# Kernel tuning notes

Measured on AMD Instinct MI355X. Metric: run time of the kernel, lower is better.

The kernel has to match this reference:

```python
import jax, jax.numpy as jnp
import numpy as np

B, S, E = 2, 2048, 1024
H, HKV = 16, 4
D = E // H          # head_dim = 64
REP = H // HKV      # kv repeat factor = 4


def setup_inputs() -> dict:
    key = jax.random.key(0)
    ks = jax.random.split(key, 9)
    std = 0.02
    x = jax.random.normal(ks[0], (B, S, E), dtype=jnp.float32)
    # causal mask: True means masked (upper triangle, strictly above diagonal)
    mask = jnp.triu(jnp.ones((S, S), dtype=bool), k=1)
    wq_w = jax.random.normal(ks[1], (E, E), dtype=jnp.float32) * std
    wq_b = jax.random.normal(ks[2], (E,), dtype=jnp.float32) * std
    wk_w = jax.random.normal(ks[3], (HKV * D, E), dtype=jnp.float32) * std
    wk_b = jax.random.normal(ks[4], (HKV * D,), dtype=jnp.float32) * std
    wv_w = jax.random.normal(ks[5], (HKV * D, E), dtype=jnp.float32) * std
    wv_b = jax.random.normal(ks[6], (HKV * D,), dtype=jnp.float32) * std
    wo_w = jax.random.normal(ks[7], (E, E), dtype=jnp.float32) * std
    wo_b = jax.random.normal(ks[8], (E,), dtype=jnp.float32) * std
    return {"x": x, "mask": mask, "wq_w": wq_w, "wq_b": wq_b,
            "wk_w": wk_w, "wk_b": wk_b, "wv_w": wv_w, "wv_b": wv_b,
            "wo_w": wo_w, "wo_b": wo_b}


def reference(x, mask, wq_w, wq_b, wk_w, wk_b, wv_w, wv_b, wo_w, wo_b):
    b, s, e = x.shape
    # projections (torch Linear: x @ W.T + b)
    q = x @ wq_w.T + wq_b                       # [B,S,E]
    k = x @ wk_w.T + wk_b                       # [B,S,HKV*D]
    v = x @ wv_w.T + wv_b
    # q grouped by kv head: [B, HKV, REP, S, D]; k/v: [B, HKV, S, D]
    q = q.reshape(b, s, HKV, REP, D).transpose(0, 2, 3, 1, 4)
    k = k.reshape(b, s, HKV, D).transpose(0, 2, 1, 3)
    v = v.reshape(b, s, HKV, D).transpose(0, 2, 1, 3)
    scale = D ** (-0.5)
    # scores [B, HKV, REP, Sq, Skv] -- same math as physical repeat_kv
    scores = jnp.einsum('bgrsd,bgtd->bgrst', q, k) * scale
    scores = jnp.where(mask, -jnp.inf, scores)
    w = jax.nn.softmax(scores, axis=-1)
    ctx = jnp.einsum('bgrst,bgtd->bgrsd', w, v)  # [B,HKV,REP,S,D]
    ctx = ctx.transpose(0, 3, 1, 2, 4).reshape(b, s, e)
    return ctx @ wo_w.T + wo_b
```

## Files before the change

### kernel.cpp

```cpp
#include <hip/hip_runtime.h>


typedef __attribute__((ext_vector_type(8))) short bh8;
typedef __attribute__((ext_vector_type(4))) short sh4;
typedef __attribute__((ext_vector_type(4))) float fv4;
typedef __attribute__((ext_vector_type(2))) unsigned int uv2;

#define MFMA16 __builtin_amdgcn_mfma_f32_16x16x32_bf16

static __device__ __forceinline__ float fast_exp2(float x) {
  return __builtin_amdgcn_exp2f(x);
}
static __device__ __forceinline__ unsigned short f2bf(float f) {
  unsigned int u; __builtin_memcpy(&u, &f, 4);
  u += 0x7fffu + ((u >> 16) & 1u);
  return (unsigned short)(u >> 16);
}
static __device__ __forceinline__ unsigned int pack2(float a, float b) {
  unsigned int r;
  asm("v_cvt_pk_bf16_f32 %0, %1, %2" : "=v"(r) : "v"(a), "v"(b));
  return r;
}
static __device__ __forceinline__ void gload16(const short* g, short* l) {
  __builtin_amdgcn_global_load_lds(
      (const __attribute__((address_space(1))) void*)g,
      (__attribute__((address_space(3))) void*)l, 16, 0, 0);
}

static __device__ __forceinline__ bh8 pshuf(const float* p, int quad, int l16) {
  unsigned int u01 = pack2(p[0], p[1]);
  unsigned int u23 = pack2(p[2], p[3]);
  unsigned int u45 = pack2(p[4], p[5]);
  unsigned int u67 = pack2(p[6], p[7]);
  const int g0 = (((quad << 1)    ) & 3) * 16 + l16;
  const int g1 = (((quad << 1) + 1) & 3) * 16 + l16;
  unsigned int w0l = __shfl((int)u01, g0), w0h = __shfl((int)u45, g0);
  unsigned int w1l = __shfl((int)u23, g0), w1h = __shfl((int)u67, g0);
  unsigned int w2l = __shfl((int)u01, g1), w2h = __shfl((int)u45, g1);
  unsigned int w3l = __shfl((int)u23, g1), w3h = __shfl((int)u67, g1);
  const bool up = (quad & 2) != 0;
  union { unsigned int w[4]; bh8 v; } pu;
  pu.w[0] = up ? w0h : w0l;
  pu.w[1] = up ? w1h : w1l;
  pu.w[2] = up ? w2h : w2l;
  pu.w[3] = up ? w3h : w3l;
  return pu.v;
}

__global__ __launch_bounds__(256) void cvt_all(
    const float* __restrict__ x,  const float* __restrict__ wq,
    const float* __restrict__ wk, const float* __restrict__ wv,
    const float* __restrict__ wo,
    short* __restrict__ xb, short* __restrict__ wqkvb, short* __restrict__ wob)
{
  const int i = blockIdx.x * 256 + threadIdx.x;
  const float* src; short* dst; int j;
  if (i < 1048576)      { j = i;           src = x;  dst = xb; }
  else if (i < 1310720) { j = i - 1048576; src = wq; dst = wqkvb; }
  else if (i < 1376256) { j = i - 1310720; src = wk; dst = wqkvb + (size_t)1024 * 1024; }
  else if (i < 1441792) { j = i - 1376256; src = wv; dst = wqkvb + (size_t)1280 * 1024; }
  else                  { j = i - 1441792; src = wo; dst = wob; }
  const float4 v = ((const float4*)src)[j];
  sh4 o = { (short)f2bf(v.x), (short)f2bf(v.y),
            (short)f2bf(v.z), (short)f2bf(v.w) };
  ((sh4*)dst)[j] = o;
}

__global__ __launch_bounds__(256) void gemm_dbuf(
    const short* __restrict__ A, const short* __restrict__ W,
    const float* __restrict__ biasQ, const float* __restrict__ biasK,
    const float* __restrict__ biasV,
    short* __restrict__ Cq, short* __restrict__ Ck, short* __restrict__ Cvt,
    float* __restrict__ Cf,
    int M, int K, int S, int mode, float scaleQ)
{
  __shared__ short As[2][128 * 64];
  __shared__ short Bs[2][64 * 64];
  const int tid  = threadIdx.x;
  const int wave = tid >> 6, lane = tid & 63;
  const int quad = lane >> 4, l16 = lane & 15;
  const int row0 = blockIdx.x * 128, col0 = blockIdx.y * 64;
  const int wr = (wave >> 1) * 64, wc = (wave & 1) * 32;

  fv4 acc[4][2] = {};

  const int srow = lane >> 3;
  const int scg  = (lane & 7) ^ srow;
  const short* ag = A + (size_t)(row0 + wave * 32 + srow) * K + scg * 8;
  const short* bg = W + (size_t)(col0 + wave * 16 + srow) * K + scg * 8;

  auto stage = [&](int b, int k0) {
    #pragma unroll
    for (int e = 0; e < 4; e++)
      gload16(ag + (size_t)(e * 8) * K + k0, &As[b][(wave * 32 + e * 8) * 64]);
    #pragma unroll
    for (int e = 0; e < 2; e++)
      gload16(bg + (size_t)(e * 8) * K + k0, &Bs[b][(wave * 16 + e * 8) * 64]);
  };

  stage(0, 0);
  __syncthreads();
  const int nIter = K / 64;
  for (int it = 0; it < nIter; it++) {
    const int cur = it & 1;
    if (it + 1 < nIter) stage(cur ^ 1, (it + 1) * 64);

    #pragma unroll
    for (int kk = 0; kk < 2; kk++) {
      const int g = kk * 4 + quad;
      bh8 af[4], bf[2];
      #pragma unroll
      for (int i = 0; i < 4; i++) {
        const int r = wr + i * 16 + l16;
        af[i] = *(const bh8*)&As[cur][r * 64 + ((g ^ (r & 7)) * 8)];
      }
      #pragma unroll
      for (int j = 0; j < 2; j++) {
        const int r = wc + j * 16 + l16;
        bf[j] = *(const bh8*)&Bs[cur][r * 64 + ((g ^ (r & 7)) * 8)];
      }
      #pragma unroll
      for (int i = 0; i < 4; i++)
        #pragma unroll
        for (int j = 0; j < 2; j++)
          acc[i][j] = MFMA16(af[i], bf[j], acc[i][j], 0, 0, 0);
    }
    __syncthreads();
  }

  if (mode == 2) {
    float bv[2];
    #pragma unroll
    for (int j = 0; j < 2; j++) bv[j] = biasQ[col0 + wc + j * 16 + l16];
    #pragma unroll
    for (int i = 0; i < 4; i++) {
      const int row = row0 + wr + i * 16 + quad * 4;
      #pragma unroll
      for (int j = 0; j < 2; j++) {
        const int col = col0 + wc + j * 16 + l16;
        #pragma unroll
        for (int r = 0; r < 4; r++)
          Cf[(size_t)(row + r) * 1024 + col] = acc[i][j][r] + bv[j];
      }
    }
  } else if (col0 < 1024) {
    float bv[2];
    #pragma unroll
    for (int j = 0; j < 2; j++) bv[j] = biasQ[col0 + wc + j * 16 + l16];
    #pragma unroll
    for (int i = 0; i < 4; i++) {
      const int row = row0 + wr + i * 16 + quad * 4;
      #pragma unroll
      for (int j = 0; j < 2; j++) {
        const int col = col0 + wc + j * 16 + l16;
        #pragma unroll
        for (int r = 0; r < 4; r++)
          Cq[(size_t)(row + r) * 1024 + col] =
              (short)f2bf((acc[i][j][r] + bv[j]) * scaleQ);
      }
    }
  } else if (col0 < 1280) {
    float bv[2];
    #pragma unroll
    for (int j = 0; j < 2; j++) bv[j] = biasK[col0 + wc + j * 16 + l16 - 1024];
    #pragma unroll
    for (int i = 0; i < 4; i++) {
      const int row = row0 + wr + i * 16 + quad * 4;
      #pragma unroll
      for (int j = 0; j < 2; j++) {
        const int col = col0 + wc + j * 16 + l16 - 1024;
        #pragma unroll
        for (int r = 0; r < 4; r++)
          Ck[(size_t)(row + r) * 256 + col] = (short)f2bf(acc[i][j][r] + bv[j]);
      }
    }
  } else {
    float bv[2];
    #pragma unroll
    for (int j = 0; j < 2; j++) bv[j] = biasV[col0 + wc + j * 16 + l16 - 1280];
    const int b  = row0 / S;
    const int sb = row0 - b * S;
    #pragma unroll
    for (int i = 0; i < 4; i++) {
      const int s = sb + wr + i * 16 + quad * 4;
      #pragma unroll
      for (int j = 0; j < 2; j++) {
        const int np = col0 + wc + j * 16 + l16 - 1280;
        sh4 v = { (short)f2bf(acc[i][j][0] + bv[j]),
                  (short)f2bf(acc[i][j][1] + bv[j]),
                  (short)f2bf(acc[i][j][2] + bv[j]),
                  (short)f2bf(acc[i][j][3] + bv[j]) };
        *(sh4*)(Cvt + ((size_t)(b * 256 + np)) * S + s) = v;
      }
    }
  }
}

__global__ __launch_bounds__(256) void gqa_attn(
    const short* __restrict__ Q,
    const short* __restrict__ Kg,
    const short* __restrict__ Vt,
    short* __restrict__ ctx)
{
  const int S = 2048, E = 1024, KVE = 256;
  __shared__ short Ks[2][4096];
  __shared__ short Vs[2][4096];
  __shared__ short P2[4][16 * 64];

  const int wave = threadIdx.x >> 6;
  const int lane = threadIdx.x & 63;
  const int quad = lane >> 4, l16 = lane & 15;
  const int bh = blockIdx.y;
  const int b = bh >> 4, h = bh & 15, kv = h >> 2;

  const short* Kb = Kg + (size_t)b * S * KVE + kv * 64;
  const short* Vb = Vt + ((size_t)(b * 4 + kv)) * 64 * S;
  short* Pw = &P2[wave][0];

  const int srow = lane >> 3;
  const int scg  = (lane & 7) ^ srow;

  const int kc0 = (quad ^ (l16 & 7)) * 8;
  const int kc1 = ((quad ^ 4) ^ (l16 & 7)) * 8;
  const int l7  = l16 & 7;
  const int pwr = l16 * 64;
  const int prA = pwr + ((quad ^ l7) * 8);
  const int prB = pwr + (((4 + quad) ^ l7) * 8);

  auto stageKV = [&](int buf, int t0) {
    #pragma unroll
    for (int e = 0; e < 2; e++) {
      const int g = wave * 2 + e;
      const int row = g * 8 + srow;
      gload16(Kb + (size_t)(t0 + row) * KVE + scg * 8, &Ks[buf][g * 512]);
      gload16(Vb + (size_t)row * S + t0 + scg * 8,     &Vs[buf][g * 512]);
    }
  };

  for (int ph = 0; ph < 2; ph++) {
    const int j = ph ? (31 - (int)blockIdx.x) : (int)blockIdx.x;
    const int qblk0 = j * 64;
    const int q0 = qblk0 + wave * 16;

    const short* qrow = Q + (size_t)(b * S + q0 + l16) * E + h * 64 + quad * 8;
    bh8 qf0 = *(const bh8*)(qrow);
    bh8 qf1 = *(const bh8*)(qrow + 32);

    fv4 acc0{}, acc1{}, acc2{}, acc3{};
    float rs = 0.f;

    const int nInt = qblk0 >> 6;
    if (nInt > 0) {
      stageKV(0, 0);
      __syncthreads();
      for (int it = 0; it < nInt; it++) {
        const int cur = it & 1;
        if (it + 1 < nInt) stageKV(cur ^ 1, (it + 1) * 64);

        fv4 st[4] = {};
        __builtin_amdgcn_s_setprio(1);
        #pragma unroll
        for (int i = 0; i < 4; i++) {
          const int tb = (i * 16 + l16) * 64;
          bh8 k0 = *(const bh8*)&Ks[cur][tb + kc0];
          bh8 k1 = *(const bh8*)&Ks[cur][tb + kc1];
          st[i] = MFMA16(k0, qf0, st[i], 0, 0, 0);
          st[i] = MFMA16(k1, qf1, st[i], 0, 0, 0);
        }
        __builtin_amdgcn_s_setprio(0);
        #pragma unroll
        for (int i = 0; i < 4; i++) {
          float p0 = fast_exp2(st[i][0]);
          float p1 = fast_exp2(st[i][1]);
          float p2 = fast_exp2(st[i][2]);
          float p3 = fast_exp2(st[i][3]);
          rs += (p0 + p1) + (p2 + p3);
          uv2 u = { pack2(p0, p1), pack2(p2, p3) };
          const int pg = ((i * 2 + (quad >> 1)) ^ l7) * 8 + (quad & 1) * 4;
          *(uv2*)&Pw[pwr + pg] = u;
        }
        bh8 pfA = *(const bh8*)&Pw[prA];
        bh8 pfB = *(const bh8*)&Pw[prB];
        __builtin_amdgcn_s_setprio(1);
        #pragma unroll
        for (int dt = 0; dt < 4; dt++) {
          const int db = (dt * 16 + l16) * 64;
          bh8 v0 = *(const bh8*)&Vs[cur][db + kc0];
          bh8 v1 = *(const bh8*)&Vs[cur][db + kc1];
          fv4* a = dt == 0 ? &acc0 : dt == 1 ? &acc1 : dt == 2 ? &acc2 : &acc3;
          *a = MFMA16(v0, pfA, *a, 0, 0, 0);
          *a = MFMA16(v1, pfB, *a, 0, 0, 0);
        }
        __builtin_amdgcn_s_setprio(0);
        __syncthreads();
      }
    }

    const int nk = q0 + 16;
    for (int t0 = qblk0; t0 < nk; t0 += 32) {
      fv4 st0{}, st1{};
      {
        const short* kr = Kb + (size_t)(t0 + l16) * KVE + quad * 8;
        bh8 k0 = *(const bh8*)(kr);
        bh8 k1 = *(const bh8*)(kr + 32);
        st0 = MFMA16(k0, qf0, st0, 0, 0, 0);
        st0 = MFMA16(k1, qf1, st0, 0, 0, 0);
      }
      const bool do2 = (t0 + 16) < nk;
      if (do2) {
        const short* kr = Kb + (size_t)(t0 + 16 + l16) * KVE + quad * 8;
        bh8 k0 = *(const bh8*)(kr);
        bh8 k1 = *(const bh8*)(kr + 32);
        st1 = MFMA16(k0, qf0, st1, 0, 0, 0);
        st1 = MFMA16(k1, qf1, st1, 0, 0, 0);
      }
      const int qg = q0 + l16;
      float p[8];
      #pragma unroll
      for (int r = 0; r < 4; r++) {
        const int t = t0 + quad * 4 + r;
        p[r]     = (t <= qg)               ? fast_exp2(st0[r]) : 0.f;
        p[4 + r] = (do2 && (t + 16) <= qg) ? fast_exp2(st1[r]) : 0.f;
      }
      #pragma unroll
      for (int i = 0; i < 8; i++) rs += p[i];

      bh8 pf = pshuf(p, quad, l16);
      const short* vr = Vb + (size_t)l16 * S + t0 + quad * 8;
      acc0 = MFMA16(*(const bh8*)(vr),          pf, acc0, 0, 0, 0);
      acc1 = MFMA16(*(const bh8*)(vr + 16 * S), pf, acc1, 0, 0, 0);
      acc2 = MFMA16(*(const bh8*)(vr + 32 * S), pf, acc2, 0, 0, 0);
      acc3 = MFMA16(*(const bh8*)(vr + 48 * S), pf, acc3, 0, 0, 0);
    }

    float lsum = rs;
    lsum += __shfl_xor(lsum, 16);
    lsum += __shfl_xor(lsum, 32);
    const float inv = 1.f / lsum;

    short* orow = ctx + (size_t)(b * S + q0 + l16) * E + h * 64 + quad * 4;
    sh4 o0 = { (short)f2bf(acc0[0] * inv), (short)f2bf(acc0[1] * inv),
               (short)f2bf(acc0[2] * inv), (short)f2bf(acc0[3] * inv) };
    sh4 o1 = { (short)f2bf(acc1[0] * inv), (short)f2bf(acc1[1] * inv),
               (short)f2bf(acc1[2] * inv), (short)f2bf(acc1[3] * inv) };
    sh4 o2 = { (short)f2bf(acc2[0] * inv), (short)f2bf(acc2[1] * inv),
               (short)f2bf(acc2[2] * inv), (short)f2bf(acc2[3] * inv) };
    sh4 o3 = { (short)f2bf(acc3[0] * inv), (short)f2bf(acc3[1] * inv),
               (short)f2bf(acc3[2] * inv), (short)f2bf(acc3[3] * inv) };
    *(sh4*)(orow)      = o0;
    *(sh4*)(orow + 16) = o1;
    *(sh4*)(orow + 32) = o2;
    *(sh4*)(orow + 48) = o3;
  }
}

extern "C" void kernel_launch(void* const* d_in, const int* in_sizes, int n_in,
                              void* d_out, int out_size, void* d_ws, size_t ws_size,
                              hipStream_t stream)
{
  const float* x    = (const float*)d_in[0];
  const float* wq_w = (const float*)d_in[2];
  const float* wq_b = (const float*)d_in[3];
  const float* wk_w = (const float*)d_in[4];
  const float* wk_b = (const float*)d_in[5];
  const float* wv_w = (const float*)d_in[6];
  const float* wv_b = (const float*)d_in[7];
  const float* wo_w = (const float*)d_in[8];
  const float* wo_b = (const float*)d_in[9];
  float* out = (float*)d_out;

  const int S = 2048, E = 1024, M = 2 * S;
  const float sl2e = 0.125f * 1.44269504f;

  char* ob = (char*)d_out;
  short* Qb   = (short*)(ob);
  short* Kbuf = (short*)(ob + (size_t)( 8 << 20));
  short* Vtb  = (short*)(ob + (size_t)(10 << 20));

  char* ws = (char*)d_ws;
  short* xb    = (short*)(ws);
  short* wqkvb = (short*)(ws + (size_t)( 8 << 20));
  short* wob   = (short*)(ws + (size_t)(11 << 20));
  short* Cx    = xb;

  dim3 blk(256);
  cvt_all<<<dim3(6656), blk, 0, stream>>>(x, wq_w, wk_w, wv_w, wo_w,
                                          xb, wqkvb, wob);
  gemm_dbuf<<<dim3(M / 128, 1536 / 64), blk, 0, stream>>>(
      xb, wqkvb, wq_b, wk_b, wv_b, Qb, Kbuf, Vtb, nullptr, M, E, S, 0, sl2e);
  gqa_attn<<<dim3(16, 2 * 16), blk, 0, stream>>>(Qb, Kbuf, Vtb, Cx);
  gemm_dbuf<<<dim3(M / 128, 1024 / 64), blk, 0, stream>>>(
      Cx, wob, wo_b, nullptr, nullptr, nullptr, nullptr, nullptr, out,
      M, E, S, 2, 1.f);
}
```

Baseline: 171.7 us.

## Process two adjacent query blocks per 512-thread workgroup sharing KV tiles

The attention kernel used to process two query blocks (j and 31-j) one after another in a 256-thread workgroup. It now runs two adjacent query blocks at once using 8 waves, and each staged K/V tile is shared by both wave groups. Each wave now stages one 8-row slice instead of two, and waves of the lower block skip compute on the last tile. This halves the K/V tile loads per query and increases parallelism per block. The trade-off is the loss of the j/31-j causal load balancing, so per-block work now varies widely, and the 512-thread blocks put more pressure on registers and occupancy.

```diff
diff --git a/kernel.cpp b/kernel.cpp
--- a/kernel.cpp
+++ b/kernel.cpp
@@ -196,7 +196,7 @@
   }
 }
 
-__global__ __launch_bounds__(256) void gqa_attn(
+__global__ __launch_bounds__(512) void gqa_attn(
     const short* __restrict__ Q,
     const short* __restrict__ Kg,
     const short* __restrict__ Vt,
@@ -205,7 +205,7 @@
   const int S = 2048, E = 1024, KVE = 256;
   __shared__ short Ks[2][4096];
   __shared__ short Vs[2][4096];
-  __shared__ short P2[4][16 * 64];
+  __shared__ short P2[8][16 * 64];
 
   const int wave = threadIdx.x >> 6;
   const int lane = threadIdx.x & 63;
@@ -228,130 +228,128 @@
   const int prB = pwr + (((4 + quad) ^ l7) * 8);
 
   auto stageKV = [&](int buf, int t0) {
-    #pragma unroll
-    for (int e = 0; e < 2; e++) {
-      const int g = wave * 2 + e;
-      const int row = g * 8 + srow;
-      gload16(Kb + (size_t)(t0 + row) * KVE + scg * 8, &Ks[buf][g * 512]);
-      gload16(Vb + (size_t)row * S + t0 + scg * 8,     &Vs[buf][g * 512]);
-    }
+    const int row = wave * 8 + srow;
+    gload16(Kb + (size_t)(t0 + row) * KVE + scg * 8, &Ks[buf][wave * 512]);
+    gload16(Vb + (size_t)row * S + t0 + scg * 8,     &Vs[buf][wave * 512]);
   };
 
-  for (int ph = 0; ph < 2; ph++) {
-    const int j = ph ? (31 - (int)blockIdx.x) : (int)blockIdx.x;
-    const int qblk0 = j * 64;
-    const int q0 = qblk0 + wave * 16;
-
-    const short* qrow = Q + (size_t)(b * S + q0 + l16) * E + h * 64 + quad * 8;
-    bh8 qf0 = *(const bh8*)(qrow);
-    bh8 qf1 = *(const bh8*)(qrow + 32);
-
-    fv4 acc0{}, acc1{}, acc2{}, acc3{};
-    float rs = 0.f;
-
-    const int nInt = qblk0 >> 6;
-    if (nInt > 0) {
-      stageKV(0, 0);
-      __syncthreads();
-      for (int it = 0; it < nInt; it++) {
-        const int cur = it & 1;
-        if (it + 1 < nInt) stageKV(cur ^ 1, (it + 1) * 64);
-
-        fv4 st[4] = {};
-        __builtin_amdgcn_s_setprio(1);
-        #pragma unroll
-        for (int i = 0; i < 4; i++) {
-          const int tb = (i * 16 + l16) * 64;
-          bh8 k0 = *(const bh8*)&Ks[cur][tb + kc0];
-          bh8 k1 = *(const bh8*)&Ks[cur][tb + kc1];
-          st[i] = MFMA16(k0, qf0, st[i], 0, 0, 0);
-          st[i] = MFMA16(k1, qf1, st[i], 0, 0, 0);
-        }
-        __builtin_amdgcn_s_setprio(0);
-        #pragma unroll
-        for (int i = 0; i < 4; i++) {
-          float p0 = fast_exp2(st[i][0]);
-          float p1 = fast_exp2(st[i][1]);
-          float p2 = fast_exp2(st[i][2]);
-          float p3 = fast_exp2(st[i][3]);
-          rs += (p0 + p1) + (p2 + p3);
-          uv2 u = { pack2(p0, p1), pack2(p2, p3) };
-          const int pg = ((i * 2 + (quad >> 1)) ^ l7) * 8 + (quad & 1) * 4;
-          *(uv2*)&Pw[pwr + pg] = u;
-        }
-        bh8 pfA = *(const bh8*)&Pw[prA];
-        bh8 pfB = *(const bh8*)&Pw[prB];
-        __builtin_amdgcn_s_setprio(1);
-        #pragma unroll
-        for (int dt = 0; dt < 4; dt++) {
-          const int db = (dt * 16 + l16) * 64;
-          bh8 v0 = *(const bh8*)&Vs[cur][db + kc0];
-          bh8 v1 = *(const bh8*)&Vs[cur][db + kc1];
-          fv4* a = dt == 0 ? &acc0 : dt == 1 ? &acc1 : dt == 2 ? &acc2 : &acc3;
-          *a = MFMA16(v0, pfA, *a, 0, 0, 0);
-          *a = MFMA16(v1, pfB, *a, 0, 0, 0);
-        }
-        __builtin_amdgcn_s_setprio(0);
-        __syncthreads();
-      }
-    }
-
-    const int nk = q0 + 16;
-    for (int t0 = qblk0; t0 < nk; t0 += 32) {
-      fv4 st0{}, st1{};
-      {
-        const short* kr = Kb + (size_t)(t0 + l16) * KVE + quad * 8;
-        bh8 k0 = *(const bh8*)(kr);
-        bh8 k1 = *(const bh8*)(kr + 32);
-        st0 = MFMA16(k0, qf0, st0, 0, 0, 0);
-        st0 = MFMA16(k1, qf1, st0, 0, 0, 0);
-      }
-      const bool do2 = (t0 + 16) < nk;
-      if (do2) {
-        const short* kr = Kb + (size_t)(t0 + 16 + l16) * KVE + quad * 8;
-        bh8 k0 = *(const bh8*)(kr);
-        bh8 k1 = *(const bh8*)(kr + 32);
-        st1 = MFMA16(k0, qf0, st1, 0, 0, 0);
-        st1 = MFMA16(k1, qf1, st1, 0, 0, 0);
-      }
-      const int qg = q0 + l16;
-      float p[8];
-      #pragma unroll
-      for (int r = 0; r < 4; r++) {
-        const int t = t0 + quad * 4 + r;
-        p[r]     = (t <= qg)               ? fast_exp2(st0[r]) : 0.f;
-        p[4 + r] = (do2 && (t + 16) <= qg) ? fast_exp2(st1[r]) : 0.f;
-      }
-      #pragma unroll
-      for (int i = 0; i < 8; i++) rs += p[i];
-
-      bh8 pf = pshuf(p, quad, l16);
-      const short* vr = Vb + (size_t)l16 * S + t0 + quad * 8;
-      acc0 = MFMA16(*(const bh8*)(vr),          pf, acc0, 0, 0, 0);
-      acc1 = MFMA16(*(const bh8*)(vr + 16 * S), pf, acc1, 0, 0, 0);
-      acc2 = MFMA16(*(const bh8*)(vr + 32 * S), pf, acc2, 0, 0, 0);
-      acc3 = MFMA16(*(const bh8*)(vr + 48 * S), pf, acc3, 0, 0, 0);
-    }
-
-    float lsum = rs;
-    lsum += __shfl_xor(lsum, 16);
-    lsum += __shfl_xor(lsum, 32);
-    const float inv = 1.f / lsum;
-
-    short* orow = ctx + (size_t)(b * S + q0 + l16) * E + h * 64 + quad * 4;
-    sh4 o0 = { (short)f2bf(acc0[0] * inv), (short)f2bf(acc0[1] * inv),
-               (short)f2bf(acc0[2] * inv), (short)f2bf(acc0[3] * inv) };
-    sh4 o1 = { (short)f2bf(acc1[0] * inv), (short)f2bf(acc1[1] * inv),
-               (short)f2bf(acc1[2] * inv), (short)f2bf(acc1[3] * inv) };
-    sh4 o2 = { (short)f2bf(acc2[0] * inv), (short)f2bf(acc2[1] * inv),
-               (short)f2bf(acc2[2] * inv), (short)f2bf(acc2[3] * inv) };
-    sh4 o3 = { (short)f2bf(acc3[0] * inv), (short)f2bf(acc3[1] * inv),
-               (short)f2bf(acc3[2] * inv), (short)f2bf(acc3[3] * inv) };
-    *(sh4*)(orow)      = o0;
-    *(sh4*)(orow + 16) = o1;
-    *(sh4*)(orow + 32) = o2;
-    *(sh4*)(orow + 48) = o3;
+  const int jbase = (15 - (int)blockIdx.x) * 2;
+  const int wg = wave >> 2;
+  const int wv = wave & 3;
+  const int j  = jbase + wg;
+  const int qblk0 = j * 64;
+  const int q0 = qblk0 + wv * 16;
+  const int nInt = j;
+  const int nmax = jbase + 1;
+
+  const short* qrow = Q + (size_t)(b * S + q0 + l16) * E + h * 64 + quad * 8;
+  bh8 qf0 = *(const bh8*)(qrow);
+  bh8 qf1 = *(const bh8*)(qrow + 32);
+
+  fv4 acc0{}, acc1{}, acc2{}, acc3{};
+  float rs = 0.f;
+
+  stageKV(0, 0);
+  __syncthreads();
+  for (int it = 0; it < nmax; it++) {
+    const int cur = it & 1;
+    if (it + 1 < nmax) stageKV(cur ^ 1, (it + 1) * 64);
+
+    if (it < nInt) {
+      fv4 st[4] = {};
+      __builtin_amdgcn_s_setprio(1);
+      #pragma unroll
+      for (int i = 0; i < 4; i++) {
+        const int tb = (i * 16 + l16) * 64;
+        bh8 k0 = *(const bh8*)&Ks[cur][tb + kc0];
+        bh8 k1 = *(const bh8*)&Ks[cur][tb + kc1];
+        st[i] = MFMA16(k0, qf0, st[i], 0, 0, 0);
+        st[i] = MFMA16(k1, qf1, st[i], 0, 0, 0);
+      }
+      __builtin_amdgcn_s_setprio(0);
+      #pragma unroll
+      for (int i = 0; i < 4; i++) {
+        float p0 = fast_exp2(st[i][0]);
+        float p1 = fast_exp2(st[i][1]);
+        float p2 = fast_exp2(st[i][2]);
+        float p3 = fast_exp2(st[i][3]);
+        rs += (p0 + p1) + (p2 + p3);
+        uv2 u = { pack2(p0, p1), pack2(p2, p3) };
+        const int pg = ((i * 2 + (quad >> 1)) ^ l7) * 8 + (quad & 1) * 4;
+        *(uv2*)&Pw[pwr + pg] = u;
+      }
+      bh8 pfA = *(const bh8*)&Pw[prA];
+      bh8 pfB = *(const bh8*)&Pw[prB];
+      __builtin_amdgcn_s_setprio(1);
+      #pragma unroll
+      for (int dt = 0; dt < 4; dt++) {
+        const int db = (dt * 16 + l16) * 64;
+        bh8 v0 = *(const bh8*)&Vs[cur][db + kc0];
+        bh8 v1 = *(const bh8*)&Vs[cur][db + kc1];
+        fv4* a = dt == 0 ? &acc0 : dt == 1 ? &acc1 : dt == 2 ? &acc2 : &acc3;
+        *a = MFMA16(v0, pfA, *a, 0, 0, 0);
+        *a = MFMA16(v1, pfB, *a, 0, 0, 0);
+      }
+      __builtin_amdgcn_s_setprio(0);
+    }
+    __syncthreads();
   }
+
+  const int nk = q0 + 16;
+  for (int t0 = qblk0; t0 < nk; t0 += 32) {
+    fv4 st0{}, st1{};
+    {
+      const short* kr = Kb + (size_t)(t0 + l16) * KVE + quad * 8;
+      bh8 k0 = *(const bh8*)(kr);
+      bh8 k1 = *(const bh8*)(kr + 32);
+      st0 = MFMA16(k0, qf0, st0, 0, 0, 0);
+      st0 = MFMA16(k1, qf1, st0, 0, 0, 0);
+    }
+    const bool do2 = (t0 + 16) < nk;
+    if (do2) {
+      const short* kr = Kb + (size_t)(t0 + 16 + l16) * KVE + quad * 8;
+      bh8 k0 = *(const bh8*)(kr);
+      bh8 k1 = *(const bh8*)(kr + 32);
+      st1 = MFMA16(k0, qf0, st1, 0, 0, 0);
+      st1 = MFMA16(k1, qf1, st1, 0, 0, 0);
+    }
+    const int qg = q0 + l16;
+    float p[8];
+    #pragma unroll
+    for (int r = 0; r < 4; r++) {
+      const int t = t0 + quad * 4 + r;
+      p[r]     = (t <= qg)               ? fast_exp2(st0[r]) : 0.f;
+      p[4 + r] = (do2 && (t + 16) <= qg) ? fast_exp2(st1[r]) : 0.f;
+    }
+    #pragma unroll
+    for (int i = 0; i < 8; i++) rs += p[i];
+
+    bh8 pf = pshuf(p, quad, l16);
+    const short* vr = Vb + (size_t)l16 * S + t0 + quad * 8;
+    acc0 = MFMA16(*(const bh8*)(vr),          pf, acc0, 0, 0, 0);
+    acc1 = MFMA16(*(const bh8*)(vr + 16 * S), pf, acc1, 0, 0, 0);
+    acc2 = MFMA16(*(const bh8*)(vr + 32 * S), pf, acc2, 0, 0, 0);
+    acc3 = MFMA16(*(const bh8*)(vr + 48 * S), pf, acc3, 0, 0, 0);
+  }
+
+  float lsum = rs;
+  lsum += __shfl_xor(lsum, 16);
+  lsum += __shfl_xor(lsum, 32);
+  const float inv = 1.f / lsum;
+
+  short* orow = ctx + (size_t)(b * S + q0 + l16) * E + h * 64 + quad * 4;
+  sh4 o0 = { (short)f2bf(acc0[0] * inv), (short)f2bf(acc0[1] * inv),
+             (short)f2bf(acc0[2] * inv), (short)f2bf(acc0[3] * inv) };
+  sh4 o1 = { (short)f2bf(acc1[0] * inv), (short)f2bf(acc1[1] * inv),
+             (short)f2bf(acc1[2] * inv), (short)f2bf(acc1[3] * inv) };
+  sh4 o2 = { (short)f2bf(acc2[0] * inv), (short)f2bf(acc2[1] * inv),
+             (short)f2bf(acc2[2] * inv), (short)f2bf(acc2[3] * inv) };
+  sh4 o3 = { (short)f2bf(acc3[0] * inv), (short)f2bf(acc3[1] * inv),
+             (short)f2bf(acc3[2] * inv), (short)f2bf(acc3[3] * inv) };
+  *(sh4*)(orow)      = o0;
+  *(sh4*)(orow + 16) = o1;
+  *(sh4*)(orow + 32) = o2;
+  *(sh4*)(orow + 48) = o3;
 }
 
 extern "C" void kernel_launch(void* const* d_in, const int* in_sizes, int n_in,
@@ -388,7 +386,7 @@
                                           xb, wqkvb, wob);
   gemm_dbuf<<<dim3(M / 128, 1536 / 64), blk, 0, stream>>>(
       xb, wqkvb, wq_b, wk_b, wv_b, Qb, Kbuf, Vtb, nullptr, M, E, S, 0, sl2e);
-  gqa_attn<<<dim3(16, 2 * 16), blk, 0, stream>>>(Qb, Kbuf, Vtb, Cx);
+  gqa_attn<<<dim3(16, 2 * 16), dim3(512), 0, stream>>>(Qb, Kbuf, Vtb, Cx);
   gemm_dbuf<<<dim3(M / 128, 1024 / 64), blk, 0, stream>>>(
       Cx, wob, wo_b, nullptr, nullptr, nullptr, nullptr, nullptr, out,
       M, E, S, 2, 1.f);
```

Measured after the change: 176.3 us. 1.03x slower.
